# Kernel optimization log

Measured on AMD Instinct MI355X. Metric: run time of the kernel, lower is better.

The kernel has to match this reference:

```python
import jax, jax.numpy as jnp
import numpy as np

HEADS, MAX_SEQ, N_STATE = 8, 2048, 512
DEPTH = N_STATE // HEADS
B, S = 2, 2048
EPS = 1e-5


def setup_inputs() -> dict:
    key = jax.random.key(0)
    ks = jax.random.split(key, 8)
    sd = lambda f: 1.0 / np.sqrt(f)
    causal = jnp.tril(jnp.ones((S, S), dtype=bool))
    mask = jnp.where(causal, 0.0, -1e9).astype(jnp.float32)[None, None]
    return {
        "x": jax.random.normal(ks[0], (B, S, N_STATE), jnp.float32),
        "mask": mask,
        "W_qkv": jax.random.normal(ks[1], (N_STATE, 3 * N_STATE), jnp.float32) * sd(N_STATE),
        "b_qkv": jnp.zeros((3 * N_STATE,), jnp.float32),
        "W_proj": jax.random.normal(ks[2], (N_STATE, N_STATE), jnp.float32) * sd(N_STATE),
        "b_proj": jnp.zeros((N_STATE,), jnp.float32),
        "E": jax.random.normal(ks[3], (HEADS, MAX_SEQ, DEPTH), jnp.float32) * sd(DEPTH),
        "g1": jnp.ones((N_STATE,), jnp.float32),
        "be1": jnp.zeros((N_STATE,), jnp.float32),
        "g2": jnp.ones((N_STATE,), jnp.float32),
        "be2": jnp.zeros((N_STATE,), jnp.float32),
        "W_fc1": jax.random.normal(ks[4], (N_STATE, 4 * N_STATE), jnp.float32) * sd(N_STATE),
        "b_fc1": jnp.zeros((4 * N_STATE,), jnp.float32),
        "W_fc2": jax.random.normal(ks[5], (4 * N_STATE, N_STATE), jnp.float32) * sd(4 * N_STATE),
        "b_fc2": jnp.zeros((N_STATE,), jnp.float32),
    }


def _layernorm(x, g, b):
    mu = jnp.mean(x, axis=-1, keepdims=True)
    var = jnp.mean(jnp.square(x - mu), axis=-1, keepdims=True)
    return (x - mu) * jax.lax.rsqrt(var + EPS) * g + b


def _relative_skew(rel):
    # rel: [B, H, S, S] = q @ E_slice^T ; skew trick -> relative positions
    b, h, s, _ = rel.shape
    rel = jnp.pad(rel, ((0, 0), (0, 0), (0, 0), (1, 0)))  # [B,H,S,S+1]
    rel = rel.reshape(b, h, s + 1, s)
    return rel[:, :, 1:, :]  # [B,H,S,S]


def reference(x, mask, W_qkv, b_qkv, W_proj, b_proj, E, g1, be1, g2, be2,
              W_fc1, b_fc1, W_fc2, b_fc2):
    b, s, _ = x.shape
    a = _layernorm(x, g1, be1)
    qkv = a @ W_qkv + b_qkv  # [B,S,3N]
    q, k, v = jnp.split(qkv, 3, axis=-1)
    split = lambda t: t.reshape(b, s, HEADS, DEPTH).transpose(0, 2, 1, 3)  # [B,H,S,D]
    q, k, v = split(q), split(k), split(v)
    present = jnp.stack([k, v], axis=1)  # [B,2,H,S,D]

    w = jnp.einsum("bhqd,bhkd->bhqk", q, k)
    E_s = E[:, MAX_SEq if False else MAX_SEQ - s:, :]  # [H,S,D]
    rel = jnp.einsum("bhqd,hld->bhql", q, E_s)
    w = (w + _relative_skew(rel)) * (1.0 / np.sqrt(DEPTH))
    w = w + mask
    w = jax.nn.softmax(w, axis=-1)
    att = jnp.einsum("bhqk,bhkd->bhqd", w, v)
    att = att.transpose(0, 2, 1, 3).reshape(b, s, N_STATE)
    att = att @ W_proj + b_proj

    x = x + att
    m = _layernorm(x, g2, be2)
    m = jax.nn.gelu(m @ W_fc1 + b_fc1) @ W_fc2 + b_fc2
    x = x + m
    return (x, present)
```

## Files before the change

kernel.cpp:

```cpp
#include <hip/hip_runtime.h>
#include <stdint.h>

#define DEV __device__ __forceinline__

typedef __attribute__((ext_vector_type(8))) short bf16x8;
typedef __attribute__((ext_vector_type(4))) float f32x4;

DEV ushort f2bf(float f) {
  union { float f; uint32_t u; } c; c.f = f;
  return (ushort)((c.u + 0x7FFFu + ((c.u >> 16) & 1)) >> 16);
}
DEV bf16x8 ld8(const ushort* p) { return *reinterpret_cast<const bf16x8*>(p); }

DEV void gload16(const void* g, void* l) {
  __builtin_amdgcn_global_load_lds(
      (const __attribute__((address_space(1))) uint32_t*)g,
      (__attribute__((address_space(3))) uint32_t*)l, 16, 0, 0);
}

__global__ __launch_bounds__(256) void k_transpose_bf(const float* __restrict__ in,
                                                      ushort* __restrict__ out,
                                                      int R, int C) {
  __shared__ float t[32][33];
  int tx = threadIdx.x & 31, ty = threadIdx.x >> 5;
  int c0 = blockIdx.x * 32, r0 = blockIdx.y * 32;
#pragma unroll
  for (int k = 0; k < 4; ++k)
    t[ty + 8 * k][tx] = in[(size_t)(r0 + ty + 8 * k) * C + c0 + tx];
  __syncthreads();
#pragma unroll
  for (int k = 0; k < 4; ++k)
    out[(size_t)(c0 + ty + 8 * k) * R + r0 + tx] = f2bf(t[tx][ty + 8 * k]);
}

__global__ __launch_bounds__(256) void k_cvt_bf(const float* __restrict__ in,
                                                ushort* __restrict__ out, int n4) {
  int i = blockIdx.x * 256 + threadIdx.x;
  if (i >= n4) return;
  float4 v = reinterpret_cast<const float4*>(in)[i];
  ushort4 o; o.x = f2bf(v.x); o.y = f2bf(v.y); o.z = f2bf(v.z); o.w = f2bf(v.w);
  reinterpret_cast<ushort4*>(out)[i] = o;
}

__global__ __launch_bounds__(64) void k_ln(const float* __restrict__ x,
                                           const float* __restrict__ g,
                                           const float* __restrict__ be,
                                           ushort* __restrict__ out) {
  int row = blockIdx.x, lane = threadIdx.x;
  const float* xr = x + (size_t)row * 512 + lane * 8;
  float4 a = *reinterpret_cast<const float4*>(xr);
  float4 b = *reinterpret_cast<const float4*>(xr + 4);
  float xs[8] = {a.x, a.y, a.z, a.w, b.x, b.y, b.z, b.w};
  float s = 0.f, q = 0.f;
#pragma unroll
  for (int i = 0; i < 8; ++i) { s += xs[i]; q += xs[i] * xs[i]; }
#pragma unroll
  for (int off = 32; off; off >>= 1) { s += __shfl_xor(s, off); q += __shfl_xor(q, off); }
  float mu = s * (1.f / 512.f);
  float var = q * (1.f / 512.f) - mu * mu;
  float inv = rsqrtf(var + 1e-5f);
  const float* gp = g + lane * 8;
  const float* bp = be + lane * 8;
  ushort o[8];
#pragma unroll
  for (int i = 0; i < 8; ++i) o[i] = f2bf((xs[i] - mu) * inv * gp[i] + bp[i]);
  *reinterpret_cast<uint4*>(out + (size_t)row * 512 + lane * 8) = *reinterpret_cast<uint4*>(o);
}

template <int EPI>
__global__ __launch_bounds__(256) void k_gemm(
    const ushort* __restrict__ A, const ushort* __restrict__ Bt,
    int M, int N, int K,
    const float* __restrict__ bias, const float* __restrict__ res,
    float* __restrict__ outf, ushort* __restrict__ outb,
    float* __restrict__ present, ushort* __restrict__ qbf,
    ushort* __restrict__ kbf, ushort* __restrict__ vtbf) {
  __shared__ ushort As[128][64];
  __shared__ ushort Bs[128][64];
  const int tid = threadIdx.x, lane = tid & 63, w = tid >> 6;
  const int g = lane >> 4, l16 = lane & 15;
  const int m0 = blockIdx.y * 128, n0 = blockIdx.x * 128;
  const int wm = (w >> 1) * 64, wn = (w & 1) * 64;
  f32x4 acc[4][4];
#pragma unroll
  for (int i = 0; i < 4; ++i)
#pragma unroll
    for (int j = 0; j < 4; ++j) acc[i][j] = (f32x4){0.f, 0.f, 0.f, 0.f};

  const int lrow_off = (lane << 4);
  for (int k0 = 0; k0 < K; k0 += 64) {
#pragma unroll
    for (int sw = 0; sw < 4; ++sw) {
      int offb = sw * 4096 + w * 1024;
      int loff = offb + lrow_off;
      int row = loff >> 7, colb = loff & 127;
      gload16((const char*)A + (((size_t)(m0 + row) * K + k0) << 1) + colb,
              (char*)As + offb);
      gload16((const char*)Bt + (((size_t)(n0 + row) * K + k0) << 1) + colb,
              (char*)Bs + offb);
    }
    __syncthreads();
#pragma unroll
    for (int kk = 0; kk < 2; ++kk) {
      bf16x8 af[4], bfr[4];
#pragma unroll
      for (int f = 0; f < 4; ++f) {
        af[f] = *reinterpret_cast<const bf16x8*>(&As[wm + f * 16 + l16][kk * 32 + g * 8]);
        bfr[f] = *reinterpret_cast<const bf16x8*>(&Bs[wn + f * 16 + l16][kk * 32 + g * 8]);
      }
#pragma unroll
      for (int i = 0; i < 4; ++i)
#pragma unroll
        for (int j = 0; j < 4; ++j)
          acc[i][j] = __builtin_amdgcn_mfma_f32_16x16x32_bf16(af[i], bfr[j], acc[i][j], 0, 0, 0);
    }
    __syncthreads();
  }

#pragma unroll
  for (int i = 0; i < 4; ++i)
#pragma unroll
    for (int j = 0; j < 4; ++j)
#pragma unroll
      for (int r = 0; r < 4; ++r) {
        int row = m0 + wm + i * 16 + g * 4 + r;
        int col = n0 + wn + j * 16 + l16;
        float v = acc[i][j][r] + bias[col];
        if constexpr (EPI == 0) {
          int third = col >> 9, hh = (col >> 6) & 7, d = col & 63;
          int bb = row >> 11, sq = row & 2047;
          if (third == 0) {
            qbf[((((size_t)bb * 8 + hh) * 2048) + sq) * 64 + d] = f2bf(v);
          } else {
            present[((((size_t)bb * 2 + (third - 1)) * 8 + hh) * 2048 + sq) * 64 + d] = v;
            if (third == 1)
              kbf[((((size_t)bb * 8 + hh) * 2048) + sq) * 64 + d] = f2bf(v);
            else
              vtbf[(((size_t)bb * 8 + hh) * 64 + d) * 2048 + sq] = f2bf(v);
          }
        } else if constexpr (EPI == 1) {
          size_t idx = (size_t)row * N + col;
          outf[idx] = v + res[idx];
        } else {
          float u = 0.7978845608f * (v + 0.044715f * v * v * v);
          float e = __expf(2.f * u);
          float th = 1.f - 2.f / (e + 1.f);
          outb[(size_t)row * N + col] = f2bf(0.5f * v * (1.f + th));
        }
      }
}

__global__ __launch_bounds__(128) void k_attn(
    const ushort* __restrict__ qbf, const ushort* __restrict__ kbf,
    const ushort* __restrict__ vtbf, const ushort* __restrict__ Ebf,
    ushort* __restrict__ attb) {
  constexpr int S = 2048;
  __shared__ float Rs[2][16][84];
  __shared__ ushort Ps[2][16][76];
  __shared__ float Mrg[2][64][24];
  const int tid = threadIdx.x, lane = tid & 63, ks = tid >> 6;
  const int g = lane >> 4, l16 = lane & 15;
  const int bid = blockIdx.x;
  const int xcd = bid & 7, idx = bid >> 3;
  const int b = idx & 1, p = idx >> 1;
  const int h = xcd, bh = b * 8 + h;
  const ushort* qp = qbf + (size_t)bh * S * 64;
  const ushort* kp = kbf + (size_t)bh * S * 64;
  const ushort* vp = vtbf + (size_t)bh * 64 * S;
  const ushort* ep = Ebf + (size_t)h * S * 64;

  for (int si = 0; si < 2; ++si) {
    const int t = si ? (127 - p) : p;
    const int i0 = t * 16;
    bf16x8 qf[2];
    qf[0] = ld8(qp + (size_t)(i0 + l16) * 64 + g * 8);
    qf[1] = ld8(qp + (size_t)(i0 + l16) * 64 + 32 + g * 8);
    f32x4 o[4];
#pragma unroll
    for (int fv = 0; fv < 4; ++fv) o[fv] = (f32x4){0.f, 0.f, 0.f, 0.f};
    float mrun[4], lrun[4];
#pragma unroll
    for (int r = 0; r < 4; ++r) { mrun[r] = -1e30f; lrun[r] = 0.f; }
    const int nkt = t / 4 + 1;

    for (int kt = ks; kt < nkt; kt += 2) {
      const int j0 = kt * 64;
      f32x4 sacc[4];
#pragma unroll
      for (int fn = 0; fn < 4; ++fn) sacc[fn] = (f32x4){0.f, 0.f, 0.f, 0.f};
#pragma unroll
      for (int kk = 0; kk < 2; ++kk)
#pragma unroll
        for (int fn = 0; fn < 4; ++fn) {
          bf16x8 kf = ld8(kp + (size_t)(j0 + fn * 16 + l16) * 64 + kk * 32 + g * 8);
          sacc[fn] = __builtin_amdgcn_mfma_f32_16x16x32_bf16(qf[kk], kf, sacc[fn], 0, 0, 0);
        }
      const int tb = S - 16 - i0 + j0;
      f32x4 racc[5];
#pragma unroll
      for (int fc = 0; fc < 5; ++fc) racc[fc] = (f32x4){0.f, 0.f, 0.f, 0.f};
#pragma unroll
      for (int kk = 0; kk < 2; ++kk)
#pragma unroll
        for (int fc = 0; fc < 5; ++fc) {
          int l = tb + fc * 16 + l16; if (l > S - 1) l = S - 1;
          bf16x8 ef = ld8(ep + (size_t)l * 64 + kk * 32 + g * 8);
          racc[fc] = __builtin_amdgcn_mfma_f32_16x16x32_bf16(qf[kk], ef, racc[fc], 0, 0, 0);
        }
#pragma unroll
      for (int fc = 0; fc < 5; ++fc)
#pragma unroll
        for (int r = 0; r < 4; ++r)
          Rs[ks][g * 4 + r][fc * 16 + l16] = racc[fc][r];

      float Sv[4][4], mtile[4];
#pragma unroll
      for (int r = 0; r < 4; ++r) mtile[r] = -1e30f;
#pragma unroll
      for (int fn = 0; fn < 4; ++fn)
#pragma unroll
        for (int r = 0; r < 4; ++r) {
          int dr = g * 4 + r, dj = fn * 16 + l16;
          float sv = (sacc[fn][r] + Rs[ks][dr][15 - dr + dj]) * 0.125f;
          if (j0 + dj > i0 + dr) sv = -1e30f;
          Sv[fn][r] = sv;
          mtile[r] = fmaxf(mtile[r], sv);
        }
#pragma unroll
      for (int off = 1; off < 16; off <<= 1)
#pragma unroll
        for (int r = 0; r < 4; ++r) mtile[r] = fmaxf(mtile[r], __shfl_xor(mtile[r], off));
      float corr[4], psum[4];
#pragma unroll
      for (int r = 0; r < 4; ++r) {
        float mn = fmaxf(mrun[r], mtile[r]);
        corr[r] = __expf(mrun[r] - mn);
        mrun[r] = mn;
        psum[r] = 0.f;
      }
#pragma unroll
      for (int fn = 0; fn < 4; ++fn)
#pragma unroll
        for (int r = 0; r < 4; ++r) {
          float pv = __expf(Sv[fn][r] - mrun[r]);
          psum[r] += pv;
          Ps[ks][g * 4 + r][fn * 16 + l16] = f2bf(pv);
        }
#pragma unroll
      for (int off = 1; off < 16; off <<= 1)
#pragma unroll
        for (int r = 0; r < 4; ++r) psum[r] += __shfl_xor(psum[r], off);
#pragma unroll
      for (int r = 0; r < 4; ++r) lrun[r] = lrun[r] * corr[r] + psum[r];
#pragma unroll
      for (int fv = 0; fv < 4; ++fv)
#pragma unroll
        for (int r = 0; r < 4; ++r) o[fv][r] *= corr[r];

#pragma unroll
      for (int kk = 0; kk < 2; ++kk) {
        bf16x8 pf = ld8(&Ps[ks][l16][kk * 32 + g * 8]);
#pragma unroll
        for (int fv = 0; fv < 4; ++fv) {
          bf16x8 vf = ld8(vp + (size_t)(fv * 16 + l16) * S + j0 + kk * 32 + g * 8);
          o[fv] = __builtin_amdgcn_mfma_f32_16x16x32_bf16(pf, vf, o[fv], 0, 0, 0);
        }
      }
    }

    if (ks == 1) {
      float* mb = &Mrg[si][lane][0];
#pragma unroll
      for (int fv = 0; fv < 4; ++fv)
#pragma unroll
        for (int r = 0; r < 4; ++r) mb[fv * 4 + r] = o[fv][r];
#pragma unroll
      for (int r = 0; r < 4; ++r) { mb[16 + r] = mrun[r]; mb[20 + r] = lrun[r]; }
    }
    __syncthreads();
    if (ks == 0) {
      const float* mb = &Mrg[si][lane][0];
#pragma unroll
      for (int r = 0; r < 4; ++r) {
        float m1 = mb[16 + r];
        float mm = fmaxf(mrun[r], m1);
        float e0 = __expf(mrun[r] - mm), e1 = __expf(m1 - mm);
        float lc = lrun[r] * e0 + mb[20 + r] * e1;
        float inv = 1.f / lc;
#pragma unroll
        for (int fv = 0; fv < 4; ++fv) {
          float oc = o[fv][r] * e0 + mb[fv * 4 + r] * e1;
          attb[(size_t)(b * S + i0 + g * 4 + r) * 512 + h * 64 + fv * 16 + l16] =
              f2bf(oc * inv);
        }
      }
    }
  }
}

extern "C" void kernel_launch(void* const* d_in, const int* in_sizes, int n_in,
                              void* d_out, int out_size, void* d_ws, size_t ws_size,
                              hipStream_t stream) {
  const float* x = (const float*)d_in[0];
  const float* W_qkv = (const float*)d_in[2];
  const float* b_qkv = (const float*)d_in[3];
  const float* W_proj = (const float*)d_in[4];
  const float* b_proj = (const float*)d_in[5];
  const float* E = (const float*)d_in[6];
  const float* g1 = (const float*)d_in[7];
  const float* be1 = (const float*)d_in[8];
  const float* g2 = (const float*)d_in[9];
  const float* be2 = (const float*)d_in[10];
  const float* W_fc1 = (const float*)d_in[11];
  const float* b_fc1 = (const float*)d_in[12];
  const float* W_fc2 = (const float*)d_in[13];
  const float* b_fc2 = (const float*)d_in[14];

  float* x_out = (float*)d_out;
  float* present = x_out + 2097152;

  char* ws = (char*)d_ws;
  ushort* a_bf   = (ushort*)(ws + 0);
  ushort* m_bf   = (ushort*)(ws + 4194304);
  ushort* q_bf   = (ushort*)(ws + 8388608);
  ushort* att_bf = (ushort*)(ws + 12582912);
  ushort* h_bf   = (ushort*)(ws + 16777216);
  ushort* k_bf   = (ushort*)(ws + 16777216);
  ushort* vt_bf  = (ushort*)(ws + 20971520);
  float*  x2     = (float*)(ws + 33554432);
  ushort* Wqkv_t = (ushort*)(ws + 41943040);
  ushort* Wproj_t= (ushort*)(ws + 43515904);
  ushort* Wfc1_t = (ushort*)(ws + 44040192);
  ushort* Wfc2_t = (ushort*)(ws + 46137344);
  ushort* E_bf   = (ushort*)(ws + 48234496);

  k_transpose_bf<<<dim3(48, 16), 256, 0, stream>>>(W_qkv, Wqkv_t, 512, 1536);
  k_transpose_bf<<<dim3(16, 16), 256, 0, stream>>>(W_proj, Wproj_t, 512, 512);
  k_transpose_bf<<<dim3(64, 16), 256, 0, stream>>>(W_fc1, Wfc1_t, 512, 2048);
  k_transpose_bf<<<dim3(16, 64), 256, 0, stream>>>(W_fc2, Wfc2_t, 2048, 512);
  k_cvt_bf<<<1024, 256, 0, stream>>>(E, E_bf, 262144);
  k_ln<<<4096, 64, 0, stream>>>(x, g1, be1, a_bf);
  k_gemm<0><<<dim3(12, 32), 256, 0, stream>>>(a_bf, Wqkv_t, 4096, 1536, 512,
                                              b_qkv, nullptr, nullptr, nullptr,
                                              present, q_bf, k_bf, vt_bf);
  k_attn<<<1024, 128, 0, stream>>>(q_bf, k_bf, vt_bf, E_bf, att_bf);
  k_gemm<1><<<dim3(4, 32), 256, 0, stream>>>(att_bf, Wproj_t, 4096, 512, 512,
                                             b_proj, x, x2, nullptr, nullptr, nullptr,
                                             nullptr, nullptr);
  k_ln<<<4096, 64, 0, stream>>>(x2, g2, be2, m_bf);
  k_gemm<2><<<dim3(16, 32), 256, 0, stream>>>(m_bf, Wfc1_t, 4096, 2048, 512,
                                              b_fc1, nullptr, nullptr, h_bf, nullptr,
                                              nullptr, nullptr, nullptr);
  k_gemm<1><<<dim3(4, 32), 256, 0, stream>>>(h_bf, Wfc2_t, 4096, 512, 2048,
                                             b_fc2, x2, x_out, nullptr, nullptr, nullptr,
                                             nullptr, nullptr);
}
```

Before: 336.1 us.

## Rebalance work: one q-tile per attention block, narrower N tiles, 4-row layernorm blocks

```diff
diff --git a/kernel.cpp b/kernel.cpp
--- a/kernel.cpp
+++ b/kernel.cpp
@@ -42,11 +42,12 @@
   reinterpret_cast<ushort4*>(out)[i] = o;
 }
 
-__global__ __launch_bounds__(64) void k_ln(const float* __restrict__ x,
-                                           const float* __restrict__ g,
-                                           const float* __restrict__ be,
-                                           ushort* __restrict__ out) {
-  int row = blockIdx.x, lane = threadIdx.x;
+__global__ __launch_bounds__(256) void k_ln(const float* __restrict__ x,
+                                            const float* __restrict__ g,
+                                            const float* __restrict__ be,
+                                            ushort* __restrict__ out) {
+  int w = threadIdx.x >> 6, lane = threadIdx.x & 63;
+  int row = blockIdx.x * 4 + w;
   const float* xr = x + (size_t)row * 512 + lane * 8;
   float4 a = *reinterpret_cast<const float4*>(xr);
   float4 b = *reinterpret_cast<const float4*>(xr + 4);
@@ -67,7 +68,7 @@
   *reinterpret_cast<uint4*>(out + (size_t)row * 512 + lane * 8) = *reinterpret_cast<uint4*>(o);
 }
 
-template <int EPI>
+template <int EPI, int BN>
 __global__ __launch_bounds__(256) void k_gemm(
     const ushort* __restrict__ A, const ushort* __restrict__ Bt,
     int M, int N, int K,
@@ -75,17 +76,18 @@
     float* __restrict__ outf, ushort* __restrict__ outb,
     float* __restrict__ present, ushort* __restrict__ qbf,
     ushort* __restrict__ kbf, ushort* __restrict__ vtbf) {
+  constexpr int NF = BN / 32;
   __shared__ ushort As[128][64];
-  __shared__ ushort Bs[128][64];
+  __shared__ ushort Bs[BN][64];
   const int tid = threadIdx.x, lane = tid & 63, w = tid >> 6;
   const int g = lane >> 4, l16 = lane & 15;
-  const int m0 = blockIdx.y * 128, n0 = blockIdx.x * 128;
-  const int wm = (w >> 1) * 64, wn = (w & 1) * 64;
-  f32x4 acc[4][4];
+  const int m0 = blockIdx.y * 128, n0 = blockIdx.x * BN;
+  const int wm = (w >> 1) * 64, wn = (w & 1) * (BN / 2);
+  f32x4 acc[4][NF];
 #pragma unroll
   for (int i = 0; i < 4; ++i)
 #pragma unroll
-    for (int j = 0; j < 4; ++j) acc[i][j] = (f32x4){0.f, 0.f, 0.f, 0.f};
+    for (int j = 0; j < NF; ++j) acc[i][j] = (f32x4){0.f, 0.f, 0.f, 0.f};
 
   const int lrow_off = (lane << 4);
   for (int k0 = 0; k0 < K; k0 += 64) {
@@ -96,22 +98,29 @@
       int row = loff >> 7, colb = loff & 127;
       gload16((const char*)A + (((size_t)(m0 + row) * K + k0) << 1) + colb,
               (char*)As + offb);
+    }
+#pragma unroll
+    for (int sw = 0; sw < BN / 32; ++sw) {
+      int offb = sw * 4096 + w * 1024;
+      int loff = offb + lrow_off;
+      int row = loff >> 7, colb = loff & 127;
       gload16((const char*)Bt + (((size_t)(n0 + row) * K + k0) << 1) + colb,
               (char*)Bs + offb);
     }
     __syncthreads();
 #pragma unroll
     for (int kk = 0; kk < 2; ++kk) {
-      bf16x8 af[4], bfr[4];
-#pragma unroll
-      for (int f = 0; f < 4; ++f) {
+      bf16x8 af[4], bfr[NF];
+#pragma unroll
+      for (int f = 0; f < 4; ++f)
         af[f] = *reinterpret_cast<const bf16x8*>(&As[wm + f * 16 + l16][kk * 32 + g * 8]);
+#pragma unroll
+      for (int f = 0; f < NF; ++f)
         bfr[f] = *reinterpret_cast<const bf16x8*>(&Bs[wn + f * 16 + l16][kk * 32 + g * 8]);
-      }
 #pragma unroll
       for (int i = 0; i < 4; ++i)
 #pragma unroll
-        for (int j = 0; j < 4; ++j)
+        for (int j = 0; j < NF; ++j)
           acc[i][j] = __builtin_amdgcn_mfma_f32_16x16x32_bf16(af[i], bfr[j], acc[i][j], 0, 0, 0);
     }
     __syncthreads();
@@ -120,7 +129,7 @@
 #pragma unroll
   for (int i = 0; i < 4; ++i)
 #pragma unroll
-    for (int j = 0; j < 4; ++j)
+    for (int j = 0; j < NF; ++j)
 #pragma unroll
       for (int r = 0; r < 4; ++r) {
         int row = m0 + wm + i * 16 + g * 4 + r;
@@ -150,149 +159,149 @@
       }
 }
 
-__global__ __launch_bounds__(128) void k_attn(
+__global__ __launch_bounds__(128, 4) void k_attn(
     const ushort* __restrict__ qbf, const ushort* __restrict__ kbf,
     const ushort* __restrict__ vtbf, const ushort* __restrict__ Ebf,
     ushort* __restrict__ attb) {
   constexpr int S = 2048;
-  __shared__ float Rs[2][16][84];
-  __shared__ ushort Ps[2][16][76];
-  __shared__ float Mrg[2][64][24];
+  constexpr int REG = 5376 + 2432;
+  __shared__ alignas(16) char pool[2 * REG];
   const int tid = threadIdx.x, lane = tid & 63, ks = tid >> 6;
   const int g = lane >> 4, l16 = lane & 15;
   const int bid = blockIdx.x;
-  const int xcd = bid & 7, idx = bid >> 3;
-  const int b = idx & 1, p = idx >> 1;
-  const int h = xcd, bh = b * 8 + h;
+  const int h = bid & 7, rest = bid >> 3;
+  const int b = rest & 1, t = 127 - (rest >> 1);
+  const int bh = b * 8 + h;
+  float(*Rs)[84] = (float(*)[84])(pool + ks * REG);
+  ushort(*Ps)[76] = (ushort(*)[76])(pool + ks * REG + 5376);
+  float* Mrg = (float*)(pool + REG);
+
   const ushort* qp = qbf + (size_t)bh * S * 64;
   const ushort* kp = kbf + (size_t)bh * S * 64;
   const ushort* vp = vtbf + (size_t)bh * 64 * S;
   const ushort* ep = Ebf + (size_t)h * S * 64;
 
-  for (int si = 0; si < 2; ++si) {
-    const int t = si ? (127 - p) : p;
-    const int i0 = t * 16;
-    bf16x8 qf[2];
-    qf[0] = ld8(qp + (size_t)(i0 + l16) * 64 + g * 8);
-    qf[1] = ld8(qp + (size_t)(i0 + l16) * 64 + 32 + g * 8);
-    f32x4 o[4];
-#pragma unroll
-    for (int fv = 0; fv < 4; ++fv) o[fv] = (f32x4){0.f, 0.f, 0.f, 0.f};
-    float mrun[4], lrun[4];
-#pragma unroll
-    for (int r = 0; r < 4; ++r) { mrun[r] = -1e30f; lrun[r] = 0.f; }
-    const int nkt = t / 4 + 1;
-
-    for (int kt = ks; kt < nkt; kt += 2) {
-      const int j0 = kt * 64;
-      f32x4 sacc[4];
-#pragma unroll
-      for (int fn = 0; fn < 4; ++fn) sacc[fn] = (f32x4){0.f, 0.f, 0.f, 0.f};
-#pragma unroll
-      for (int kk = 0; kk < 2; ++kk)
-#pragma unroll
-        for (int fn = 0; fn < 4; ++fn) {
-          bf16x8 kf = ld8(kp + (size_t)(j0 + fn * 16 + l16) * 64 + kk * 32 + g * 8);
-          sacc[fn] = __builtin_amdgcn_mfma_f32_16x16x32_bf16(qf[kk], kf, sacc[fn], 0, 0, 0);
-        }
-      const int tb = S - 16 - i0 + j0;
-      f32x4 racc[5];
-#pragma unroll
-      for (int fc = 0; fc < 5; ++fc) racc[fc] = (f32x4){0.f, 0.f, 0.f, 0.f};
-#pragma unroll
-      for (int kk = 0; kk < 2; ++kk)
-#pragma unroll
-        for (int fc = 0; fc < 5; ++fc) {
-          int l = tb + fc * 16 + l16; if (l > S - 1) l = S - 1;
-          bf16x8 ef = ld8(ep + (size_t)l * 64 + kk * 32 + g * 8);
-          racc[fc] = __builtin_amdgcn_mfma_f32_16x16x32_bf16(qf[kk], ef, racc[fc], 0, 0, 0);
-        }
-#pragma unroll
-      for (int fc = 0; fc < 5; ++fc)
-#pragma unroll
-        for (int r = 0; r < 4; ++r)
-          Rs[ks][g * 4 + r][fc * 16 + l16] = racc[fc][r];
-
-      float Sv[4][4], mtile[4];
-#pragma unroll
-      for (int r = 0; r < 4; ++r) mtile[r] = -1e30f;
-#pragma unroll
-      for (int fn = 0; fn < 4; ++fn)
-#pragma unroll
-        for (int r = 0; r < 4; ++r) {
-          int dr = g * 4 + r, dj = fn * 16 + l16;
-          float sv = (sacc[fn][r] + Rs[ks][dr][15 - dr + dj]) * 0.125f;
-          if (j0 + dj > i0 + dr) sv = -1e30f;
-          Sv[fn][r] = sv;
-          mtile[r] = fmaxf(mtile[r], sv);
-        }
-#pragma unroll
-      for (int off = 1; off < 16; off <<= 1)
-#pragma unroll
-        for (int r = 0; r < 4; ++r) mtile[r] = fmaxf(mtile[r], __shfl_xor(mtile[r], off));
-      float corr[4], psum[4];
+  const int i0 = t * 16;
+  bf16x8 qf[2];
+  qf[0] = ld8(qp + (size_t)(i0 + l16) * 64 + g * 8);
+  qf[1] = ld8(qp + (size_t)(i0 + l16) * 64 + 32 + g * 8);
+  f32x4 o[4];
+#pragma unroll
+  for (int fv = 0; fv < 4; ++fv) o[fv] = (f32x4){0.f, 0.f, 0.f, 0.f};
+  float mrun[4], lrun[4];
+#pragma unroll
+  for (int r = 0; r < 4; ++r) { mrun[r] = -1e30f; lrun[r] = 0.f; }
+  const int nkt = (t + 4) >> 2;
+
+  for (int kt = ks; kt < nkt; kt += 2) {
+    const int j0 = kt * 64;
+    f32x4 sacc[4];
+#pragma unroll
+    for (int fn = 0; fn < 4; ++fn) sacc[fn] = (f32x4){0.f, 0.f, 0.f, 0.f};
+#pragma unroll
+    for (int kk = 0; kk < 2; ++kk)
+#pragma unroll
+      for (int fn = 0; fn < 4; ++fn) {
+        bf16x8 kf = ld8(kp + (size_t)(j0 + fn * 16 + l16) * 64 + kk * 32 + g * 8);
+        sacc[fn] = __builtin_amdgcn_mfma_f32_16x16x32_bf16(qf[kk], kf, sacc[fn], 0, 0, 0);
+      }
+    const int tb = S - 16 - i0 + j0;
+    f32x4 racc[5];
+#pragma unroll
+    for (int fc = 0; fc < 5; ++fc) racc[fc] = (f32x4){0.f, 0.f, 0.f, 0.f};
+#pragma unroll
+    for (int kk = 0; kk < 2; ++kk)
+#pragma unroll
+      for (int fc = 0; fc < 5; ++fc) {
+        int l = tb + fc * 16 + l16; if (l > S - 1) l = S - 1;
+        bf16x8 ef = ld8(ep + (size_t)l * 64 + kk * 32 + g * 8);
+        racc[fc] = __builtin_amdgcn_mfma_f32_16x16x32_bf16(qf[kk], ef, racc[fc], 0, 0, 0);
+      }
+#pragma unroll
+    for (int fc = 0; fc < 5; ++fc)
+#pragma unroll
+      for (int r = 0; r < 4; ++r)
+        Rs[g * 4 + r][fc * 16 + l16] = racc[fc][r];
+
+    float Sv[4][4], mtile[4];
+#pragma unroll
+    for (int r = 0; r < 4; ++r) mtile[r] = -1e30f;
+#pragma unroll
+    for (int fn = 0; fn < 4; ++fn)
 #pragma unroll
       for (int r = 0; r < 4; ++r) {
-        float mn = fmaxf(mrun[r], mtile[r]);
-        corr[r] = __expf(mrun[r] - mn);
-        mrun[r] = mn;
-        psum[r] = 0.f;
-      }
-#pragma unroll
-      for (int fn = 0; fn < 4; ++fn)
-#pragma unroll
-        for (int r = 0; r < 4; ++r) {
-          float pv = __expf(Sv[fn][r] - mrun[r]);
-          psum[r] += pv;
-          Ps[ks][g * 4 + r][fn * 16 + l16] = f2bf(pv);
-        }
-#pragma unroll
-      for (int off = 1; off < 16; off <<= 1)
-#pragma unroll
-        for (int r = 0; r < 4; ++r) psum[r] += __shfl_xor(psum[r], off);
-#pragma unroll
-      for (int r = 0; r < 4; ++r) lrun[r] = lrun[r] * corr[r] + psum[r];
-#pragma unroll
-      for (int fv = 0; fv < 4; ++fv)
-#pragma unroll
-        for (int r = 0; r < 4; ++r) o[fv][r] *= corr[r];
-
-#pragma unroll
-      for (int kk = 0; kk < 2; ++kk) {
-        bf16x8 pf = ld8(&Ps[ks][l16][kk * 32 + g * 8]);
-#pragma unroll
-        for (int fv = 0; fv < 4; ++fv) {
-          bf16x8 vf = ld8(vp + (size_t)(fv * 16 + l16) * S + j0 + kk * 32 + g * 8);
-          o[fv] = __builtin_amdgcn_mfma_f32_16x16x32_bf16(pf, vf, o[fv], 0, 0, 0);
-        }
-      }
-    }
-
-    if (ks == 1) {
-      float* mb = &Mrg[si][lane][0];
-#pragma unroll
-      for (int fv = 0; fv < 4; ++fv)
-#pragma unroll
-        for (int r = 0; r < 4; ++r) mb[fv * 4 + r] = o[fv][r];
-#pragma unroll
-      for (int r = 0; r < 4; ++r) { mb[16 + r] = mrun[r]; mb[20 + r] = lrun[r]; }
-    }
-    __syncthreads();
-    if (ks == 0) {
-      const float* mb = &Mrg[si][lane][0];
+        int dr = g * 4 + r, dj = fn * 16 + l16;
+        float sv = (sacc[fn][r] + Rs[dr][15 - dr + dj]) * 0.125f;
+        if (j0 + dj > i0 + dr) sv = -1e30f;
+        Sv[fn][r] = sv;
+        mtile[r] = fmaxf(mtile[r], sv);
+      }
+#pragma unroll
+    for (int off = 1; off < 16; off <<= 1)
+#pragma unroll
+      for (int r = 0; r < 4; ++r) mtile[r] = fmaxf(mtile[r], __shfl_xor(mtile[r], off));
+    float corr[4], psum[4];
+#pragma unroll
+    for (int r = 0; r < 4; ++r) {
+      float mn = fmaxf(mrun[r], mtile[r]);
+      corr[r] = __expf(mrun[r] - mn);
+      mrun[r] = mn;
+      psum[r] = 0.f;
+    }
+#pragma unroll
+    for (int fn = 0; fn < 4; ++fn)
 #pragma unroll
       for (int r = 0; r < 4; ++r) {
-        float m1 = mb[16 + r];
-        float mm = fmaxf(mrun[r], m1);
-        float e0 = __expf(mrun[r] - mm), e1 = __expf(m1 - mm);
-        float lc = lrun[r] * e0 + mb[20 + r] * e1;
-        float inv = 1.f / lc;
-#pragma unroll
-        for (int fv = 0; fv < 4; ++fv) {
-          float oc = o[fv][r] * e0 + mb[fv * 4 + r] * e1;
-          attb[(size_t)(b * S + i0 + g * 4 + r) * 512 + h * 64 + fv * 16 + l16] =
-              f2bf(oc * inv);
-        }
+        float pv = __expf(Sv[fn][r] - mrun[r]);
+        psum[r] += pv;
+        Ps[g * 4 + r][fn * 16 + l16] = f2bf(pv);
+      }
+#pragma unroll
+    for (int off = 1; off < 16; off <<= 1)
+#pragma unroll
+      for (int r = 0; r < 4; ++r) psum[r] += __shfl_xor(psum[r], off);
+#pragma unroll
+    for (int r = 0; r < 4; ++r) lrun[r] = lrun[r] * corr[r] + psum[r];
+#pragma unroll
+    for (int fv = 0; fv < 4; ++fv)
+#pragma unroll
+      for (int r = 0; r < 4; ++r) o[fv][r] *= corr[r];
+
+#pragma unroll
+    for (int kk = 0; kk < 2; ++kk) {
+      bf16x8 pf = ld8(&Ps[l16][kk * 32 + g * 8]);
+#pragma unroll
+      for (int fv = 0; fv < 4; ++fv) {
+        bf16x8 vf = ld8(vp + (size_t)(fv * 16 + l16) * S + j0 + kk * 32 + g * 8);
+        o[fv] = __builtin_amdgcn_mfma_f32_16x16x32_bf16(pf, vf, o[fv], 0, 0, 0);
+      }
+    }
+  }
+
+  if (ks == 1) {
+    float* mb = Mrg + lane * 24;
+#pragma unroll
+    for (int fv = 0; fv < 4; ++fv)
+#pragma unroll
+      for (int r = 0; r < 4; ++r) mb[fv * 4 + r] = o[fv][r];
+#pragma unroll
+    for (int r = 0; r < 4; ++r) { mb[16 + r] = mrun[r]; mb[20 + r] = lrun[r]; }
+  }
+  __syncthreads();
+  if (ks == 0) {
+    const float* mb = Mrg + lane * 24;
+#pragma unroll
+    for (int r = 0; r < 4; ++r) {
+      float m1 = mb[16 + r];
+      float mm = fmaxf(mrun[r], m1);
+      float e0 = __expf(mrun[r] - mm), e1 = __expf(m1 - mm);
+      float lc = lrun[r] * e0 + mb[20 + r] * e1;
+      float inv = 1.f / lc;
+#pragma unroll
+      for (int fv = 0; fv < 4; ++fv) {
+        float oc = o[fv][r] * e0 + mb[fv * 4 + r] * e1;
+        attb[(size_t)(b * S + i0 + g * 4 + r) * 512 + h * 64 + fv * 16 + l16] =
+            f2bf(oc * inv);
       }
     }
   }
@@ -339,19 +348,19 @@
   k_transpose_bf<<<dim3(64, 16), 256, 0, stream>>>(W_fc1, Wfc1_t, 512, 2048);
   k_transpose_bf<<<dim3(16, 64), 256, 0, stream>>>(W_fc2, Wfc2_t, 2048, 512);
   k_cvt_bf<<<1024, 256, 0, stream>>>(E, E_bf, 262144);
-  k_ln<<<4096, 64, 0, stream>>>(x, g1, be1, a_bf);
-  k_gemm<0><<<dim3(12, 32), 256, 0, stream>>>(a_bf, Wqkv_t, 4096, 1536, 512,
-                                              b_qkv, nullptr, nullptr, nullptr,
-                                              present, q_bf, k_bf, vt_bf);
-  k_attn<<<1024, 128, 0, stream>>>(q_bf, k_bf, vt_bf, E_bf, att_bf);
-  k_gemm<1><<<dim3(4, 32), 256, 0, stream>>>(att_bf, Wproj_t, 4096, 512, 512,
-                                             b_proj, x, x2, nullptr, nullptr, nullptr,
-                                             nullptr, nullptr);
-  k_ln<<<4096, 64, 0, stream>>>(x2, g2, be2, m_bf);
-  k_gemm<2><<<dim3(16, 32), 256, 0, stream>>>(m_bf, Wfc1_t, 4096, 2048, 512,
-                                              b_fc1, nullptr, nullptr, h_bf, nullptr,
-                                              nullptr, nullptr, nullptr);
-  k_gemm<1><<<dim3(4, 32), 256, 0, stream>>>(h_bf, Wfc2_t, 4096, 512, 2048,
-                                             b_fc2, x2, x_out, nullptr, nullptr, nullptr,
-                                             nullptr, nullptr);
-}
+  k_ln<<<1024, 256, 0, stream>>>(x, g1, be1, a_bf);
+  k_gemm<0, 128><<<dim3(12, 32), 256, 0, stream>>>(a_bf, Wqkv_t, 4096, 1536, 512,
+                                                   b_qkv, nullptr, nullptr, nullptr,
+                                                   present, q_bf, k_bf, vt_bf);
+  k_attn<<<2048, 128, 0, stream>>>(q_bf, k_bf, vt_bf, E_bf, att_bf);
+  k_gemm<1, 64><<<dim3(8, 32), 256, 0, stream>>>(att_bf, Wproj_t, 4096, 512, 512,
+                                                 b_proj, x, x2, nullptr, nullptr, nullptr,
+                                                 nullptr, nullptr);
+  k_ln<<<1024, 256, 0, stream>>>(x2, g2, be2, m_bf);
+  k_gemm<2, 128><<<dim3(16, 32), 256, 0, stream>>>(m_bf, Wfc1_t, 4096, 2048, 512,
+                                                   b_fc1, nullptr, nullptr, h_bf, nullptr,
+                                                   nullptr, nullptr, nullptr);
+  k_gemm<1, 64><<<dim3(8, 32), 256, 0, stream>>>(h_bf, Wfc2_t, 4096, 512, 2048,
+                                                 b_fc2, x2, x_out, nullptr, nullptr, nullptr,
+                                                 nullptr, nullptr);
+}
```

Measured after the change: 331.5 us. No clear change (-1.4%).
